# Kernel tuning notes

Measured on AMD Instinct MI355X. Metric: run time of the kernel, lower is better.

Reference implementation:

```python
import jax, jax.numpy as jnp
import numpy as np

N = 768
C = 256  # in_features == out_features (required by Linear(in_features+3, 1))

def _leaky(x):
    return jnp.where(x >= 0, x, 0.2 * x)

def setup_inputs() -> dict:
    key = jax.random.key(0)
    ks = jax.random.split(key, 10)
    features = jax.random.normal(ks[0], (N, C), dtype=jnp.float32)
    coordinates = jax.random.normal(ks[1], (N, 3), dtype=jnp.float32)
    adj = jax.random.uniform(ks[2], (N, N), dtype=jnp.float32)  # unused by forward, kept for signature fidelity
    # Learned params
    FC = jax.random.normal(ks[3], (C, C), dtype=jnp.float32) * (1.414 / jnp.sqrt(C))
    # Conv1d(2,1,kernel=1): weight [out=1, in=2, k=1] -> 2 scalars + bias
    fc_w = jax.random.normal(ks[4], (2,), dtype=jnp.float32) * 0.5
    fc_b = jax.random.normal(ks[5], (1,), dtype=jnp.float32) * 0.1
    sc_w = jax.random.normal(ks[6], (2,), dtype=jnp.float32) * 0.5
    sc_b = jax.random.normal(ks[7], (1,), dtype=jnp.float32) * 0.1
    # Linear(C+3, 1)
    lin_w = jax.random.normal(ks[8], (C + 3,), dtype=jnp.float32) * (1.0 / jnp.sqrt(C + 3))
    lin_b = jax.random.normal(ks[9], (1,), dtype=jnp.float32) * 0.1
    return {"features": features, "coordinates": coordinates, "adj": adj,
            "FC": FC, "fc_w": fc_w, "fc_b": fc_b, "sc_w": sc_w, "sc_b": sc_b,
            "lin_w": lin_w, "lin_b": lin_b}

def reference(features, coordinates, adj, FC, fc_w, fc_b, sc_w, sc_b, lin_w, lin_b):
    n = features.shape[0]
    f_input = features @ FC  # [N, C]
    # torch's repeat(1,N).view + repeat(N,1) builds pairs (i, j); the 1x1 Conv1d over
    # the 2 stacked channels is exactly w0*x_i + w1*x_j + b, then LeakyReLU(0.2).
    f_map = _leaky(fc_w[0] * f_input[:, None, :] + fc_w[1] * f_input[None, :, :] + fc_b[0])  # [N,N,C]
    s_map = _leaky(sc_w[0] * coordinates[:, None, :] + sc_w[1] * coordinates[None, :, :] + sc_b[0])  # [N,N,3]
    # Linear(C+3, 1) on cat([f_map, s_map], -1), then LeakyReLU -> [N, N]
    scores = _leaky(jnp.einsum('ijc,c->ij', f_map, lin_w[:f_input.shape[1]])
                    + jnp.einsum('ijk,k->ij', s_map, lin_w[f_input.shape[1]:])
                    + lin_b[0])
    attention = jax.nn.softmax(scores, axis=1)  # row softmax (dim=1)
    h_prime = attention @ f_input  # [N, C]
    return jax.nn.elu(h_prime)  # concat=True path
```

## Files before the change

kernel.cpp:

```cpp
#include <hip/hip_runtime.h>
#include <math.h>

#define NN 768
#define CC 256
#define TI 3

__device__ __forceinline__ float leaky(float x) { return x >= 0.0f ? x : 0.2f * x; }

__device__ __forceinline__ float waveMax(float v) {
    #pragma unroll
    for (int o = 32; o > 0; o >>= 1) v = fmaxf(v, __shfl_xor(v, o, 64));
    return v;
}
__device__ __forceinline__ float waveSum(float v) {
    #pragma unroll
    for (int o = 32; o > 0; o >>= 1) v += __shfl_xor(v, o, 64);
    return v;
}

__global__ __launch_bounds__(768) void k_prep(
    const float* __restrict__ features,
    const float* __restrict__ FC,
    const float* __restrict__ fc_w,
    const float* __restrict__ fc_b,
    const float* __restrict__ lin_w,
    float* __restrict__ f,
    float* __restrict__ g,
    float* __restrict__ D0,
    float* __restrict__ D1,
    float4* __restrict__ ut4)
{
    __shared__ float sA[TI * CC];
    __shared__ float sF[TI * CC];
    __shared__ float sredD[12], sredW[12];

    const int t  = threadIdx.x;
    const int r  = t >> 8;
    const int c  = t & 255;
    const int i0 = blockIdx.x * TI;

    sA[r * CC + c] = features[(i0 + r) * CC + c];
    __syncthreads();

    float a = 0.f;
    const float* fcp = FC + c;
    const float* ap  = sA + r * CC;
    #pragma unroll 8
    for (int k = 0; k < CC; ++k)
        a = fmaf(ap[k], fcp[k * CC], a);

    const float w1 = fc_w[1], b = fc_b[0];
    f[(i0 + r) * CC + c] = a;
    g[c * NN + i0 + r]   = fmaf(w1, a, b);
    sF[r * CC + c] = a;

    const float lw = lin_w[c];
    float dv = waveSum(lw * a);
    float wv = waveSum(lw);
    const int wid = t >> 6;
    if ((t & 63) == 0) { sredD[wid] = dv; sredW[wid] = wv; }
    __syncthreads();
    if (t < TI) {
        float D = sredD[t*4] + sredD[t*4+1] + sredD[t*4+2] + sredD[t*4+3];
        float W = sredW[t*4] + sredW[t*4+1] + sredW[t*4+2] + sredW[t*4+3];
        D0[i0 + t] = fc_w[0] * D;
        D1[i0 + t] = fmaf(w1, D, b * W);
    }
    if (t < CC) {
        const float w0 = fc_w[0];
        ut4[blockIdx.x * CC + t] = make_float4(w0 * sF[t],
                                               w0 * sF[CC + t],
                                               w0 * sF[2*CC + t],
                                               0.4f * lin_w[t]);
    }
}

__global__ __launch_bounds__(768) void k_attn(
    const float* __restrict__ f,
    const float* __restrict__ g,
    const float4* __restrict__ ut4,
    const float* __restrict__ D0,
    const float* __restrict__ D1,
    const float* __restrict__ coords,
    const float* __restrict__ sc_w,
    const float* __restrict__ sc_b,
    const float* __restrict__ lin_w,
    const float* __restrict__ lin_b,
    float* __restrict__ out)
{
    __shared__ float4 pp[NN];
    __shared__ float  hpart[12][TI][CC];
    __shared__ float4 sredm4[12];
    __shared__ float4 sreds4[12];

    const int t    = threadIdx.x;
    const int i0   = blockIdx.x * TI;
    const int w    = t >> 6;
    const int lane = t & 63;

    float a0 = 0.f, a1 = 0.f, a2 = 0.f;
    const float*  gp = g + t;
    const float4* up = ut4 + (size_t)blockIdx.x * CC;
    #pragma unroll 8
    for (int c = 0; c < CC; ++c) {
        float  gj = gp[c * NN];
        float4 u  = up[c];
        a0 = fmaf(u.w, fabsf(u.x + gj), a0);
        a1 = fmaf(u.w, fabsf(u.y + gj), a1);
        a2 = fmaf(u.w, fabsf(u.z + gj), a2);
    }

    const float sw0 = sc_w[0], sw1 = sc_w[1], sb = sc_b[0], lb = lin_b[0];
    const float lw30 = lin_w[CC], lw31 = lin_w[CC+1], lw32 = lin_w[CC+2];
    const float cj0 = fmaf(sw1, coords[t*3+0], sb);
    const float cj1 = fmaf(sw1, coords[t*3+1], sb);
    const float cj2 = fmaf(sw1, coords[t*3+2], sb);
    const float d1  = D1[t];
    float accs[3] = {a0, a1, a2};
    float scv[3];
    #pragma unroll
    for (int rr = 0; rr < TI; ++rr) {
        const int i = i0 + rr;
        float sd = lw30 * leaky(fmaf(sw0, coords[i*3+0], cj0))
                 + lw31 * leaky(fmaf(sw0, coords[i*3+1], cj1))
                 + lw32 * leaky(fmaf(sw0, coords[i*3+2], cj2));
        scv[rr] = leaky(accs[rr] + sd + 0.6f * (D0[i] + d1) + lb);
    }

    {
        float v0 = waveMax(scv[0]);
        float v1 = waveMax(scv[1]);
        float v2 = waveMax(scv[2]);
        if (lane == 0) sredm4[w] = make_float4(v0, v1, v2, 0.f);
    }
    __syncthreads();
    float m[TI];
    {
        float4 mm = sredm4[0];
        #pragma unroll
        for (int ww = 1; ww < 12; ++ww) {
            float4 x = sredm4[ww];
            mm.x = fmaxf(mm.x, x.x); mm.y = fmaxf(mm.y, x.y); mm.z = fmaxf(mm.z, x.z);
        }
        m[0] = mm.x; m[1] = mm.y; m[2] = mm.z;
    }
    float e0 = __expf(scv[0] - m[0]);
    float e1 = __expf(scv[1] - m[1]);
    float e2 = __expf(scv[2] - m[2]);
    pp[t] = make_float4(e0, e1, e2, 0.f);
    {
        float v0 = waveSum(e0);
        float v1 = waveSum(e1);
        float v2 = waveSum(e2);
        if (lane == 0) sreds4[w] = make_float4(v0, v1, v2, 0.f);
    }
    __syncthreads();
    float inv[TI];
    {
        float4 ss = sreds4[0];
        #pragma unroll
        for (int ww = 1; ww < 12; ++ww) {
            float4 x = sreds4[ww];
            ss.x += x.x; ss.y += x.y; ss.z += x.z;
        }
        inv[0] = 1.0f / ss.x; inv[1] = 1.0f / ss.y; inv[2] = 1.0f / ss.z;
    }

    float4 h0 = make_float4(0.f,0.f,0.f,0.f);
    float4 h1 = h0, h2 = h0;
    const float4* f4 = (const float4*)f;
    const int jb = w * 64;
    #pragma unroll 4
    for (int jj = 0; jj < 64; ++jj) {
        const int j = jb + jj;
        float4 fv = f4[(size_t)j * 64 + lane];
        float4 e  = pp[j];
        h0.x = fmaf(e.x, fv.x, h0.x); h0.y = fmaf(e.x, fv.y, h0.y);
        h0.z = fmaf(e.x, fv.z, h0.z); h0.w = fmaf(e.x, fv.w, h0.w);
        h1.x = fmaf(e.y, fv.x, h1.x); h1.y = fmaf(e.y, fv.y, h1.y);
        h1.z = fmaf(e.y, fv.z, h1.z); h1.w = fmaf(e.y, fv.w, h1.w);
        h2.x = fmaf(e.z, fv.x, h2.x); h2.y = fmaf(e.z, fv.y, h2.y);
        h2.z = fmaf(e.z, fv.z, h2.z); h2.w = fmaf(e.z, fv.w, h2.w);
    }
    *(float4*)&hpart[w][0][4*lane] = h0;
    *(float4*)&hpart[w][1][4*lane] = h1;
    *(float4*)&hpart[w][2][4*lane] = h2;
    __syncthreads();

    {
        const int r = t >> 8;
        const int c = t & 255;
        float h = 0.f;
        #pragma unroll
        for (int ww = 0; ww < 12; ++ww) h += hpart[ww][r][c];
        float v = h * inv[r];
        out[(i0 + r) * CC + c] = (v > 0.f) ? v : (__expf(v) - 1.0f);
    }
}

extern "C" void kernel_launch(void* const* d_in, const int* in_sizes, int n_in,
                              void* d_out, int out_size, void* d_ws, size_t ws_size,
                              hipStream_t stream) {
    const float* features = (const float*)d_in[0];
    const float* coords   = (const float*)d_in[1];
    const float* FC       = (const float*)d_in[3];
    const float* fc_w     = (const float*)d_in[4];
    const float* fc_b     = (const float*)d_in[5];
    const float* sc_w     = (const float*)d_in[6];
    const float* sc_b     = (const float*)d_in[7];
    const float* lin_w    = (const float*)d_in[8];
    const float* lin_b    = (const float*)d_in[9];
    float* out = (float*)d_out;

    float* f   = (float*)d_ws;
    float* g   = f   + NN*CC;
    float* D0  = g   + CC*NN;
    float* D1  = D0  + NN;
    float* pad = D1  + NN;
    float4* ut4 = (float4*)(pad + (16 - (((size_t)(pad - (float*)d_ws)) & 3)) % 16);
    {
        size_t off = (size_t)(D1 + NN) - (size_t)d_ws;
        off = (off + 15) & ~(size_t)15;
        ut4 = (float4*)((char*)d_ws + off);
    }

    k_prep<<<NN/TI, 768, 0, stream>>>(features, FC, fc_w, fc_b, lin_w, f, g, D0, D1, ut4);
    k_attn<<<NN/TI, 768, 0, stream>>>(f, g, ut4, D0, D1, coords, sc_w, sc_b,
                                      lin_w, lin_b, out);
}
```

Measured before the change: 114.1 us.

## Split attention over key chunks with split-softmax partials and a combine kernel

The attention kernel now splits the 768 key columns into 3 chunks, launching 768 blocks of 256 threads instead of 256 blocks of 768 threads. Each block writes a partial max, sum and unnormalized h to workspace, and a new combine kernel rescales the partials flash-decoding style before applying the ELU. The aim is more blocks and smaller per-block shared memory, for better occupancy and CU coverage. The cost is an extra kernel launch and the round trip of the partial h buffer (3×768×256 floats) through global memory.

```diff
diff --git a/kernel.cpp b/kernel.cpp
--- a/kernel.cpp
+++ b/kernel.cpp
@@ -4,6 +4,8 @@
 #define NN 768
 #define CC 256
 #define TI 3
+#define JC 256
+#define NJC 3
 
 __device__ __forceinline__ float leaky(float x) { return x >= 0.0f ? x : 0.2f * x; }
 
@@ -75,7 +77,7 @@
     }
 }
 
-__global__ __launch_bounds__(768) void k_attn(
+__global__ __launch_bounds__(256) void k_attn(
     const float* __restrict__ f,
     const float* __restrict__ g,
     const float4* __restrict__ ut4,
@@ -86,21 +88,27 @@
     const float* __restrict__ sc_b,
     const float* __restrict__ lin_w,
     const float* __restrict__ lin_b,
-    float* __restrict__ out)
+    float* __restrict__ hp,
+    float* __restrict__ Mp,
+    float* __restrict__ Lp)
 {
-    __shared__ float4 pp[NN];
-    __shared__ float  hpart[12][TI][CC];
-    __shared__ float4 sredm4[12];
-    __shared__ float4 sreds4[12];
+    __shared__ float4 pp[JC];
+    __shared__ float  hpart[4][TI][CC];
+    __shared__ float4 sredm4[4];
+    __shared__ float4 sreds4[4];
 
     const int t    = threadIdx.x;
-    const int i0   = blockIdx.x * TI;
+    const int it   = blockIdx.x & 255;
+    const int jc   = blockIdx.x >> 8;
+    const int i0   = it * TI;
+    const int jb   = jc * JC;
+    const int j    = jb + t;
     const int w    = t >> 6;
     const int lane = t & 63;
 
     float a0 = 0.f, a1 = 0.f, a2 = 0.f;
-    const float*  gp = g + t;
-    const float4* up = ut4 + (size_t)blockIdx.x * CC;
+    const float4* up = ut4 + (size_t)it * CC;
+    const float*  gp = g + j;
     #pragma unroll 8
     for (int c = 0; c < CC; ++c) {
         float  gj = gp[c * NN];
@@ -112,10 +120,10 @@
 
     const float sw0 = sc_w[0], sw1 = sc_w[1], sb = sc_b[0], lb = lin_b[0];
     const float lw30 = lin_w[CC], lw31 = lin_w[CC+1], lw32 = lin_w[CC+2];
-    const float cj0 = fmaf(sw1, coords[t*3+0], sb);
-    const float cj1 = fmaf(sw1, coords[t*3+1], sb);
-    const float cj2 = fmaf(sw1, coords[t*3+2], sb);
-    const float d1  = D1[t];
+    const float cj0 = fmaf(sw1, coords[j*3+0], sb);
+    const float cj1 = fmaf(sw1, coords[j*3+1], sb);
+    const float cj2 = fmaf(sw1, coords[j*3+2], sb);
+    const float d1  = D1[j];
     float accs[3] = {a0, a1, a2};
     float scv[3];
     #pragma unroll
@@ -136,13 +144,10 @@
     __syncthreads();
     float m[TI];
     {
-        float4 mm = sredm4[0];
-        #pragma unroll
-        for (int ww = 1; ww < 12; ++ww) {
-            float4 x = sredm4[ww];
-            mm.x = fmaxf(mm.x, x.x); mm.y = fmaxf(mm.y, x.y); mm.z = fmaxf(mm.z, x.z);
-        }
-        m[0] = mm.x; m[1] = mm.y; m[2] = mm.z;
+        float4 x0 = sredm4[0], x1 = sredm4[1], x2 = sredm4[2], x3 = sredm4[3];
+        m[0] = fmaxf(fmaxf(x0.x, x1.x), fmaxf(x2.x, x3.x));
+        m[1] = fmaxf(fmaxf(x0.y, x1.y), fmaxf(x2.y, x3.y));
+        m[2] = fmaxf(fmaxf(x0.z, x1.z), fmaxf(x2.z, x3.z));
     }
     float e0 = __expf(scv[0] - m[0]);
     float e1 = __expf(scv[1] - m[1]);
@@ -155,26 +160,25 @@
         if (lane == 0) sreds4[w] = make_float4(v0, v1, v2, 0.f);
     }
     __syncthreads();
-    float inv[TI];
-    {
-        float4 ss = sreds4[0];
-        #pragma unroll
-        for (int ww = 1; ww < 12; ++ww) {
-            float4 x = sreds4[ww];
-            ss.x += x.x; ss.y += x.y; ss.z += x.z;
-        }
-        inv[0] = 1.0f / ss.x; inv[1] = 1.0f / ss.y; inv[2] = 1.0f / ss.z;
+    if (t < TI) {
+        float4 s0 = sreds4[0], s1 = sreds4[1], s2 = sreds4[2], s3 = sreds4[3];
+        float l = (t == 0) ? (s0.x + s1.x + s2.x + s3.x)
+                : (t == 1) ? (s0.y + s1.y + s2.y + s3.y)
+                           : (s0.z + s1.z + s2.z + s3.z);
+        float mm = (t == 0) ? m[0] : (t == 1) ? m[1] : m[2];
+        Mp[(i0 + t) * NJC + jc] = mm;
+        Lp[(i0 + t) * NJC + jc] = l;
     }
 
     float4 h0 = make_float4(0.f,0.f,0.f,0.f);
     float4 h1 = h0, h2 = h0;
     const float4* f4 = (const float4*)f;
-    const int jb = w * 64;
+    const int jsl = w * 64;
     #pragma unroll 4
-    for (int jj = 0; jj < 64; ++jj) {
-        const int j = jb + jj;
-        float4 fv = f4[(size_t)j * 64 + lane];
-        float4 e  = pp[j];
+    for (int jx = 0; jx < 64; ++jx) {
+        const int jl = jsl + jx;
+        float4 fv = f4[(size_t)(jb + jl) * 64 + lane];
+        float4 e  = pp[jl];
         h0.x = fmaf(e.x, fv.x, h0.x); h0.y = fmaf(e.x, fv.y, h0.y);
         h0.z = fmaf(e.x, fv.z, h0.z); h0.w = fmaf(e.x, fv.w, h0.w);
         h1.x = fmaf(e.y, fv.x, h1.x); h1.y = fmaf(e.y, fv.y, h1.y);
@@ -187,15 +191,33 @@
     *(float4*)&hpart[w][2][4*lane] = h2;
     __syncthreads();
 
-    {
-        const int r = t >> 8;
-        const int c = t & 255;
-        float h = 0.f;
-        #pragma unroll
-        for (int ww = 0; ww < 12; ++ww) h += hpart[ww][r][c];
-        float v = h * inv[r];
-        out[(i0 + r) * CC + c] = (v > 0.f) ? v : (__expf(v) - 1.0f);
-    }
+    #pragma unroll
+    for (int r = 0; r < TI; ++r) {
+        float h = hpart[0][r][t] + hpart[1][r][t] + hpart[2][r][t] + hpart[3][r][t];
+        hp[((size_t)jc * NN + i0 + r) * CC + t] = h;
+    }
+}
+
+__global__ __launch_bounds__(256) void k_comb(
+    const float* __restrict__ hp,
+    const float* __restrict__ Mp,
+    const float* __restrict__ Lp,
+    float* __restrict__ out)
+{
+    const int t = threadIdx.x;
+    const int i = blockIdx.x;
+
+    float m0 = Mp[i*NJC+0], m1 = Mp[i*NJC+1], m2 = Mp[i*NJC+2];
+    float M  = fmaxf(fmaxf(m0, m1), m2);
+    float w0 = __expf(m0 - M), w1 = __expf(m1 - M), w2 = __expf(m2 - M);
+    float den = w0*Lp[i*NJC+0] + w1*Lp[i*NJC+1] + w2*Lp[i*NJC+2];
+    float inv = 1.0f / den;
+
+    float num = w0 * hp[((size_t)0*NN + i)*CC + t]
+              + w1 * hp[((size_t)1*NN + i)*CC + t]
+              + w2 * hp[((size_t)2*NN + i)*CC + t];
+    float v = num * inv;
+    out[i*CC + t] = (v > 0.f) ? v : (__expf(v) - 1.0f);
 }
 
 extern "C" void kernel_launch(void* const* d_in, const int* in_sizes, int n_in,
@@ -212,19 +234,22 @@
     const float* lin_b    = (const float*)d_in[9];
     float* out = (float*)d_out;
 
-    float* f   = (float*)d_ws;
-    float* g   = f   + NN*CC;
-    float* D0  = g   + CC*NN;
-    float* D1  = D0  + NN;
-    float* pad = D1  + NN;
-    float4* ut4 = (float4*)(pad + (16 - (((size_t)(pad - (float*)d_ws)) & 3)) % 16);
-    {
-        size_t off = (size_t)(D1 + NN) - (size_t)d_ws;
+    float* f  = (float*)d_ws;
+    float* g  = f  + NN*CC;
+    float* D0 = g  + CC*NN;
+    float* D1 = D0 + NN;
+    float* Mp = D1 + NN;
+    float* Lp = Mp + NN*NJC;
+    float* hp = Lp + NN*NJC;
+    float4* ut4;
+    {
+        size_t off = (size_t)((char*)(hp + (size_t)NJC*NN*CC) - (char*)d_ws);
         off = (off + 15) & ~(size_t)15;
         ut4 = (float4*)((char*)d_ws + off);
     }
 
     k_prep<<<NN/TI, 768, 0, stream>>>(features, FC, fc_w, fc_b, lin_w, f, g, D0, D1, ut4);
-    k_attn<<<NN/TI, 768, 0, stream>>>(f, g, ut4, D0, D1, coords, sc_w, sc_b,
-                                      lin_w, lin_b, out);
-}
+    k_attn<<<(NN/TI)*NJC, 256, 0, stream>>>(f, g, ut4, D0, D1, coords, sc_w, sc_b,
+                                            lin_w, lin_b, hp, Mp, Lp);
+    k_comb<<<NN, 256, 0, stream>>>(hp, Mp, Lp, out);
+}
```

After: 116.9 us. +2.5%, slower.
